# Kernel tuning notes

Measured on AMD Instinct MI355X. Metric: run time of the kernel, lower is better.

The kernel has to match this reference:

```python
import jax, jax.numpy as jnp
import numpy as np

DROP_I = 0.75  # input dropout prob
DROP_S = 0.25  # state dropout prob
DEPTH = 3      # recur_depth
NOISE_SEED = 42


def setup_inputs() -> dict:
    key = jax.random.key(0)
    ks = jax.random.split(key, 8)
    B, T, Din, D = 32, 2048, 512, 512
    s = 0.04  # init_scale
    u = lambda k, shape: jax.random.uniform(k, shape, jnp.float32, -s, s)
    return {
        "h0": jnp.zeros((1, D), jnp.float32),
        "seq": jax.random.normal(ks[0], (B, T, Din), jnp.float32),
        "wH": u(ks[1], (Din, D)),
        "bH": u(ks[2], (D,)),
        "wT": u(ks[3], (Din, D)),
        "bT": jnp.full((D,), -2.0, jnp.float32),  # init_T_bias
        "recurH_w": u(ks[4], (DEPTH, D, D)),
        # layer 0 has no bias in the source -> zero row is equivalent math
        "recurH_b": jnp.concatenate([jnp.zeros((1, D), jnp.float32), u(ks[5], (DEPTH - 1, D))], 0),
        "recurT_w": u(ks[6], (DEPTH, D, D)),
        "recurT_b": jnp.concatenate([jnp.zeros((1, D), jnp.float32), jnp.full((DEPTH - 1, D), -2.0, jnp.float32)], 0),
    }


def _dropout_noise(key, p_drop, shape, dtype):
    keep = 1.0 - p_drop
    return jax.random.bernoulli(key, keep, shape).astype(dtype) / keep


def _forward(h0, seq, wH, bH, wT, bT, recurH_w, recurH_b, recurT_w, recurT_b):
    B, T, Din = seq.shape
    D = wH.shape[1]
    k1, k2 = jax.random.split(jax.random.key(NOISE_SEED))
    # tied_noise=True: one input-noise mask shared by H/T paths, one state-noise mask
    noise_i = _dropout_noise(k1, DROP_I, (B, Din), seq.dtype)  # [B, Din], shared over time
    noise_s = _dropout_noise(k2, DROP_S, (B, D), seq.dtype)    # [B, D], shared over time & depth

    x = seq * noise_i[:, None, :]                              # [B, T, Din]
    i_H = jnp.einsum('btd,de->bte', x, wH) + bH                # [B, T, D]
    i_T = jnp.einsum('btd,de->bte', x, wT) + bT

    # Faithful to source: every timestep starts from H0 (state is not carried),
    # so time is a parallel axis and only the depth loop is sequential.
    s = jnp.broadcast_to(h0.reshape(1, 1, D), (B, T, D))
    for l in range(DEPTH):
        sd = s * noise_s[:, None, :]
        h_lin = jnp.einsum('btd,de->bte', sd, recurH_w[l]) + recurH_b[l]
        t_lin = jnp.einsum('btd,de->bte', sd, recurT_w[l]) + recurT_b[l]
        if l == 0:
            h_lin = h_lin + i_H
            t_lin = t_lin + i_T
        Hg = jnp.tanh(h_lin)
        Tg = jax.nn.sigmoid(t_lin)
        s = (Hg - s) * Tg + s  # highway combine
    return s  # [B, T, D]


def reference(h0, seq, wH, bH, wT, bT, recurH_w, recurH_b, recurT_w, recurT_b):
    return _forward(h0, seq, wH, bH, wT, bT, recurH_w, recurH_b, recurT_w, recurT_b)
```

## Files before the change

### kernel.cpp

```cpp
#include <hip/hip_runtime.h>
#include <stdint.h>
#include <math.h>

#define B_SZ   32
#define T_LEN  2048
#define DIN    512
#define DD     512
#define M_TOT  (B_SZ * T_LEN)
#define NTHREADS 256
#define WSZ    ((size_t)DD * DD)

typedef unsigned short u16;
typedef __attribute__((ext_vector_type(8))) short short8;
typedef __attribute__((ext_vector_type(4))) float f32x4;

__device__ __forceinline__ u16 f2bf(float f) {
  uint32_t u = __float_as_uint(f);
  uint32_t r = (u + 0x7FFFu + ((u >> 16) & 1u)) >> 16;
  return (u16)r;
}

typedef const void __attribute__((address_space(1)))* as1cp;
typedef void __attribute__((address_space(3)))* as3p;
__device__ __forceinline__ void async16(const void* g, void* l) {
  __builtin_amdgcn_global_load_lds((as1cp)(uintptr_t)g,
                                   (as3p)(uint32_t)(uintptr_t)l, 16, 0, 0);
}

__device__ __forceinline__ uint32_t rotl32(uint32_t x, int n) {
  return (x << n) | (x >> (32 - n));
}

__device__ __forceinline__ void threefry2x32(uint32_t k0, uint32_t k1,
                                             uint32_t x0, uint32_t x1,
                                             uint32_t& o0, uint32_t& o1) {
  const uint32_t ks0 = k0, ks1 = k1, ks2 = k0 ^ k1 ^ 0x1BD11BDAu;
  uint32_t v0 = x0 + ks0, v1 = x1 + ks1;
#define TF_R(r) { v0 += v1; v1 = rotl32(v1, (r)); v1 ^= v0; }
  TF_R(13) TF_R(15) TF_R(26) TF_R(6)
  v0 += ks1; v1 += ks2 + 1u;
  TF_R(17) TF_R(29) TF_R(16) TF_R(24)
  v0 += ks2; v1 += ks0 + 2u;
  TF_R(13) TF_R(15) TF_R(26) TF_R(6)
  v0 += ks0; v1 += ks1 + 3u;
  TF_R(17) TF_R(29) TF_R(16) TF_R(24)
  v0 += ks1; v1 += ks2 + 4u;
  TF_R(13) TF_R(15) TF_R(26) TF_R(6)
  v0 += ks2; v1 += ks0 + 5u;
#undef TF_R
  o0 = v0; o1 = v1;
}

__global__ void noise_kernel(float* __restrict__ noise_i, float* __restrict__ noise_s) {
  int i = blockIdx.x * blockDim.x + threadIdx.x;
  if (i >= B_SZ * DIN) return;
  uint32_t k1a, k1b, k2a, k2b;
  threefry2x32(0u, 42u, 0u, 0u, k1a, k1b);
  threefry2x32(0u, 42u, 0u, 1u, k2a, k2b);
  uint32_t b1, b2;
  threefry2x32(k1a, k1b, 0u, (uint32_t)i, b1, b2);
  noise_i[i] = (b1 < 0x40000000u) ? 4.0f : 0.0f;
  threefry2x32(k2a, k2b, 0u, (uint32_t)i, b1, b2);
  noise_s[i] = (b1 < 0xC0000000u) ? (1.0f / 0.75f) : 0.0f;
}

__global__ __launch_bounds__(256) void vec0_kernel(
    const float* __restrict__ h0, const float* __restrict__ noise_s,
    const float* __restrict__ rHw, const float* __restrict__ rHb,
    const float* __restrict__ rTw, const float* __restrict__ rTb,
    float* __restrict__ vH0, float* __restrict__ vT0) {
  __shared__ float sdv[DD];
  const int b = blockIdx.x >> 1;
  const int c = (blockIdx.x & 1) * 256 + threadIdx.x;
  for (int k = threadIdx.x; k < DD; k += 256)
    sdv[k] = h0[k] * noise_s[b * DD + k];
  __syncthreads();
  float aH = 0.f, aT = 0.f;
  for (int k = 0; k < DD; ++k) {
    float v = sdv[k];
    aH += v * rHw[(size_t)k * DD + c];
    aT += v * rTw[(size_t)k * DD + c];
  }
  vH0[b * DD + c] = aH + rHb[c];
  vT0[b * DD + c] = aT + rTb[c];
}

__global__ __launch_bounds__(256) void wt_all(
    const float* __restrict__ wH, const float* __restrict__ wT,
    const float* __restrict__ rHw, const float* __restrict__ rTw,
    u16* __restrict__ Wt) {
  __shared__ float tile[64][68];
  const int which = blockIdx.x >> 6;
  const float* W;
  switch (which) {
    case 0: W = wH; break;
    case 1: W = wT; break;
    case 2: W = rHw + WSZ; break;
    case 3: W = rTw + WSZ; break;
    case 4: W = rHw + 2 * WSZ; break;
    default: W = rTw + 2 * WSZ; break;
  }
  u16* dst = Wt + (size_t)which * WSZ;
  const int tb = blockIdx.x & 63;
  const int kt = (tb >> 3) * 64;
  const int nt = (tb & 7) * 64;
  const int tid = threadIdx.x;
  {
    int r = tid >> 2;
#pragma unroll
    for (int u = 0; u < 4; ++u) {
      int c = ((tid & 3) + u * 4) * 4;
      float4 v = *(const float4*)(W + (size_t)(kt + r) * DD + nt + c);
      tile[r][c] = v.x; tile[r][c + 1] = v.y; tile[r][c + 2] = v.z; tile[r][c + 3] = v.w;
    }
  }
  __syncthreads();
  {
    int n = tid >> 2, seg = (tid & 3) * 16;
    u16 o[16];
#pragma unroll
    for (int u = 0; u < 16; ++u) o[u] = f2bf(tile[seg + u][n]);
    *(uint4*)(dst + (size_t)(nt + n) * DD + kt + seg) = *(const uint4*)o;
    *(uint4*)(dst + (size_t)(nt + n) * DD + kt + seg + 8) = *(const uint4*)(o + 8);
  }
}

__global__ __launch_bounds__(256) void xprep(const float* __restrict__ seq,
                                             const float* __restrict__ noise_i,
                                             u16* __restrict__ Xbf) {
  int idx = blockIdx.x * 256 + threadIdx.x;
  int row = idx >> 6;
  int k8 = (idx & 63) * 8;
  int b = row >> 11;
  const float* s = seq + (size_t)row * DIN + k8;
  const float* n = noise_i + b * DIN + k8;
  float4 s0 = *(const float4*)s, s1 = *(const float4*)(s + 4);
  float4 n0 = *(const float4*)n, n1 = *(const float4*)(n + 4);
  u16 o[8];
  o[0] = f2bf(s0.x * n0.x); o[1] = f2bf(s0.y * n0.y);
  o[2] = f2bf(s0.z * n0.z); o[3] = f2bf(s0.w * n0.w);
  o[4] = f2bf(s1.x * n1.x); o[5] = f2bf(s1.y * n1.y);
  o[6] = f2bf(s1.z * n1.z); o[7] = f2bf(s1.w * n1.w);
  *(uint4*)(Xbf + (size_t)idx * 8) = *(const uint4*)o;
}

__global__ __launch_bounds__(256, 2) void layer_gemm(
    const u16* __restrict__ Abf,
    const u16* __restrict__ WtH,
    const u16* __restrict__ WtT,
    const float* __restrict__ hbv,
    const float* __restrict__ tbv,
    const float* __restrict__ vH0,
    const float* __restrict__ vT0,
    const float* __restrict__ h0,
    const float* __restrict__ noise_s,
    const float* Sprev,
    float* Snew,
    u16* __restrict__ SDnew,
    float* Out,
    int layer) {
  __shared__ u16 lds[24576];
  u16* ldsA  = lds;
  u16* ldsBH = lds + 8192;
  u16* ldsBT = lds + 16384;

  const int tid  = threadIdx.x;
  const int lane = tid & 63, wid = tid >> 6;
  const int bid  = blockIdx.x;
  const int m0   = (bid >> 2) * 128;
  const int c0   = (bid & 3) * 128;
  const int bidx = m0 >> 11;
  const int q  = lane >> 4, mr = lane & 15;
  const int wqm = wid >> 1, wqn = wid & 1;

  const u16* gA[4]; const u16* gBH[4]; const u16* gBT[4];
  u16* lA[4]; u16* lBH[4]; u16* lBT[4];
#pragma unroll
  for (int t = 0; t < 4; ++t) {
    int s  = wid * 256 + t * 64 + lane;
    int rm = s >> 3;
    int k8 = (s & 7) ^ (rm & 7);
    gA[t]  = Abf + (size_t)(m0 + rm) * DD + k8 * 8;
    gBH[t] = WtH + (size_t)(c0 + rm) * DD + k8 * 8;
    gBT[t] = WtT + (size_t)(c0 + rm) * DD + k8 * 8;
    int lofs = (wid * 256 + t * 64) * 8;
    lA[t] = ldsA + lofs; lBH[t] = ldsBH + lofs; lBT[t] = ldsBT + lofs;
  }

  f32x4 accH[4][4], accT[4][4];
#pragma unroll
  for (int i = 0; i < 4; ++i)
#pragma unroll
    for (int j = 0; j < 4; ++j) {
      accH[i][j] = (f32x4){0.f, 0.f, 0.f, 0.f};
      accT[i][j] = (f32x4){0.f, 0.f, 0.f, 0.f};
    }

  for (int kb = 0; kb < 8; ++kb) {
    __syncthreads();
    const int ko = kb * 64;
#pragma unroll
    for (int t = 0; t < 4; ++t) {
      async16(gA[t] + ko,  lA[t]);
      async16(gBH[t] + ko, lBH[t]);
      async16(gBT[t] + ko, lBT[t]);
    }
    __syncthreads();

#pragma unroll
    for (int ks = 0; ks < 2; ++ks) {
      const int jj = ((((ks << 2) + q) ^ (mr & 7)) << 3);
      short8 a[4];
#pragma unroll
      for (int mt = 0; mt < 4; ++mt)
        a[mt] = *(const short8*)(ldsA + (wqm * 64 + mt * 16 + mr) * 64 + jj);
#pragma unroll
      for (int nt = 0; nt < 4; ++nt) {
        int nofs = (wqn * 64 + nt * 16 + mr) * 64 + jj;
        short8 bh = *(const short8*)(ldsBH + nofs);
        short8 bt = *(const short8*)(ldsBT + nofs);
#pragma unroll
        for (int mt = 0; mt < 4; ++mt) {
          accH[mt][nt] = __builtin_amdgcn_mfma_f32_16x16x32_bf16(a[mt], bh, accH[mt][nt], 0, 0, 0);
          accT[mt][nt] = __builtin_amdgcn_mfma_f32_16x16x32_bf16(a[mt], bt, accT[mt][nt], 0, 0, 0);
        }
      }
    }
  }

  const int b512 = bidx * DD;
#pragma unroll
  for (int nt = 0; nt < 4; ++nt) {
    const int gc = c0 + wqn * 64 + nt * 16 + mr;
    float hb = hbv[gc], tb = tbv[gc];
    float nsc = 0.f, h0c = 0.f;
    if (layer == 0) {
      hb += vH0[b512 + gc];
      tb += vT0[b512 + gc];
      h0c = h0[gc];
    }
    if (layer < 2) nsc = noise_s[b512 + gc];
#pragma unroll
    for (int mt = 0; mt < 4; ++mt) {
      const int gmb = m0 + wqm * 64 + mt * 16 + q * 4;
#pragma unroll
      for (int r = 0; r < 4; ++r) {
        const size_t o = (size_t)(gmb + r) * DD + gc;
        float sp = (layer == 0) ? h0c : Sprev[o];
        float hg = tanhf(accH[mt][nt][r] + hb);
        float tg = 1.f / (1.f + __expf(-(accT[mt][nt][r] + tb)));
        float sn = (hg - sp) * tg + sp;
        if (layer < 2) {
          Snew[o] = sn;
          SDnew[o] = f2bf(sn * nsc);
        } else {
          Out[o] = sn;
        }
      }
    }
  }
}

extern "C" void kernel_launch(void* const* d_in, const int* in_sizes, int n_in,
                              void* d_out, int out_size, void* d_ws, size_t ws_size,
                              hipStream_t stream) {
  const float* h0  = (const float*)d_in[0];
  const float* seq = (const float*)d_in[1];
  const float* wH  = (const float*)d_in[2];
  const float* bH  = (const float*)d_in[3];
  const float* wT  = (const float*)d_in[4];
  const float* bT  = (const float*)d_in[5];
  const float* rHw = (const float*)d_in[6];
  const float* rHb = (const float*)d_in[7];
  const float* rTw = (const float*)d_in[8];
  const float* rTb = (const float*)d_in[9];
  float* out = (float*)d_out;

  char* ws = (char*)d_ws;
  float* noise_i = (float*)(ws);
  float* noise_s = (float*)(ws + (64 << 10));
  float* vH0     = (float*)(ws + (128 << 10));
  float* vT0     = (float*)(ws + (192 << 10));
  u16* Wt    = (u16*)(ws + (256 << 10));
  u16* Xbf   = (u16*)(ws + (4ull << 20));
  u16* SD0   = (u16*)(ws + (68ull << 20));

  noise_kernel<<<64, 256, 0, stream>>>(noise_i, noise_s);
  vec0_kernel<<<64, 256, 0, stream>>>(h0, noise_s, rHw, rHb, rTw, rTb, vH0, vT0);
  wt_all<<<384, 256, 0, stream>>>(wH, wT, rHw, rTw, Wt);
  xprep<<<M_TOT * DIN / 8 / 256, 256, 0, stream>>>(seq, noise_i, Xbf);

  const int NBLK = (M_TOT / 128) * (DD / 128);
  layer_gemm<<<NBLK, NTHREADS, 0, stream>>>(
      Xbf, Wt + 0 * WSZ, Wt + 1 * WSZ, bH, bT, vH0, vT0, h0, noise_s,
      nullptr, out, SD0, nullptr, 0);
  layer_gemm<<<NBLK, NTHREADS, 0, stream>>>(
      SD0, Wt + 2 * WSZ, Wt + 3 * WSZ, rHb + DD, rTb + DD, nullptr, nullptr, h0, noise_s,
      out, out, Xbf, nullptr, 1);
  layer_gemm<<<NBLK, NTHREADS, 0, stream>>>(
      Xbf, Wt + 4 * WSZ, Wt + 5 * WSZ, rHb + 2 * DD, rTb + 2 * DD, nullptr, nullptr, h0, noise_s,
      out, nullptr, nullptr, out, 2);
}
```

Before: 789.5 us.

## Triple-buffer K-loop with async LDS prefetch and swizzle block order

Replaces the single-buffered 64-wide K loop, which synchronized twice per step and waited on each load, with a 3-stage ring of 32-wide K tiles. Prefetching runs two tiles ahead and is gated by explicit vmcnt waits, so global-to-LDS copies overlap the MFMA work. It also remaps block IDs to change how tiles are spread across XCDs for L2 reuse. The cost is more LDS per block, which may affect occupancy, and the unswizzled LDS layout may introduce bank conflicts.

After: 801.4 us. Within noise of the previous version (+1.5%).

```diff
diff --git a/kernel.cpp b/kernel.cpp
--- a/kernel.cpp
+++ b/kernel.cpp
@@ -144,6 +144,9 @@
   *(uint4*)(Xbf + (size_t)idx * 8) = *(const uint4*)o;
 }
 
+#define WAITVM(n) asm volatile("s_waitcnt vmcnt(" #n ")" ::: "memory")
+#define WAITLG0() asm volatile("s_waitcnt lgkmcnt(0)" ::: "memory")
+
 __global__ __launch_bounds__(256, 2) void layer_gemm(
     const u16* __restrict__ Abf,
     const u16* __restrict__ WtH,
@@ -159,33 +162,38 @@
     u16* __restrict__ SDnew,
     float* Out,
     int layer) {
-  __shared__ u16 lds[24576];
-  u16* ldsA  = lds;
-  u16* ldsBH = lds + 8192;
-  u16* ldsBT = lds + 16384;
+  __shared__ u16 lds[36864];
 
   const int tid  = threadIdx.x;
   const int lane = tid & 63, wid = tid >> 6;
-  const int bid  = blockIdx.x;
+  const int bid  = (blockIdx.x & 7) * 256 + (blockIdx.x >> 3);
   const int m0   = (bid >> 2) * 128;
   const int c0   = (bid & 3) * 128;
   const int bidx = m0 >> 11;
   const int q  = lane >> 4, mr = lane & 15;
   const int wqm = wid >> 1, wqn = wid & 1;
 
-  const u16* gA[4]; const u16* gBH[4]; const u16* gBT[4];
-  u16* lA[4]; u16* lBH[4]; u16* lBT[4];
-#pragma unroll
-  for (int t = 0; t < 4; ++t) {
-    int s  = wid * 256 + t * 64 + lane;
-    int rm = s >> 3;
-    int k8 = (s & 7) ^ (rm & 7);
-    gA[t]  = Abf + (size_t)(m0 + rm) * DD + k8 * 8;
-    gBH[t] = WtH + (size_t)(c0 + rm) * DD + k8 * 8;
-    gBT[t] = WtT + (size_t)(c0 + rm) * DD + k8 * 8;
-    int lofs = (wid * 256 + t * 64) * 8;
-    lA[t] = ldsA + lofs; lBH[t] = ldsBH + lofs; lBT[t] = ldsBT + lofs;
-  }
+  const u16* gAb[2]; const u16* gBHb[2]; const u16* gBTb[2];
+  int lofs[2];
+#pragma unroll
+  for (int t = 0; t < 2; ++t) {
+    int g = tid + t * 256;
+    int row = g >> 2, k8 = (g & 3) * 8;
+    gAb[t]  = Abf + (size_t)(m0 + row) * DD + k8;
+    gBHb[t] = WtH + (size_t)(c0 + row) * DD + k8;
+    gBTb[t] = WtT + (size_t)(c0 + row) * DD + k8;
+    lofs[t] = g * 8;
+  }
+
+#define STAGE(bi, kb) do {                                     \
+    u16* ba = lds + (bi) * 12288;                              \
+    const int ko_ = (kb) * 32;                                 \
+    _Pragma("unroll")                                          \
+    for (int t = 0; t < 2; ++t) {                              \
+      async16(gAb[t]  + ko_, ba + lofs[t]);                    \
+      async16(gBHb[t] + ko_, ba + 4096 + lofs[t]);             \
+      async16(gBTb[t] + ko_, ba + 8192 + lofs[t]);             \
+    } } while (0)
 
   f32x4 accH[4][4], accT[4][4];
 #pragma unroll
@@ -196,37 +204,40 @@
       accT[i][j] = (f32x4){0.f, 0.f, 0.f, 0.f};
     }
 
-  for (int kb = 0; kb < 8; ++kb) {
-    __syncthreads();
-    const int ko = kb * 64;
-#pragma unroll
-    for (int t = 0; t < 4; ++t) {
-      async16(gA[t] + ko,  lA[t]);
-      async16(gBH[t] + ko, lBH[t]);
-      async16(gBT[t] + ko, lBT[t]);
-    }
-    __syncthreads();
-
-#pragma unroll
-    for (int ks = 0; ks < 2; ++ks) {
-      const int jj = ((((ks << 2) + q) ^ (mr & 7)) << 3);
-      short8 a[4];
-#pragma unroll
-      for (int mt = 0; mt < 4; ++mt)
-        a[mt] = *(const short8*)(ldsA + (wqm * 64 + mt * 16 + mr) * 64 + jj);
-#pragma unroll
-      for (int nt = 0; nt < 4; ++nt) {
-        int nofs = (wqn * 64 + nt * 16 + mr) * 64 + jj;
-        short8 bh = *(const short8*)(ldsBH + nofs);
-        short8 bt = *(const short8*)(ldsBT + nofs);
-#pragma unroll
-        for (int mt = 0; mt < 4; ++mt) {
-          accH[mt][nt] = __builtin_amdgcn_mfma_f32_16x16x32_bf16(a[mt], bh, accH[mt][nt], 0, 0, 0);
-          accT[mt][nt] = __builtin_amdgcn_mfma_f32_16x16x32_bf16(a[mt], bt, accT[mt][nt], 0, 0, 0);
-        }
+  STAGE(0, 0);
+  STAGE(1, 1);
+
+#pragma unroll
+  for (int kb = 0; kb < 16; ++kb) {
+    if (kb + 2 < 16) STAGE((kb + 2) % 3, kb + 2);
+    if (kb < 14)      WAITVM(12);
+    else if (kb == 14) WAITVM(6);
+    else               WAITVM(0);
+    __builtin_amdgcn_s_barrier();
+
+    const u16* bufA  = lds + (kb % 3) * 12288;
+    const u16* bufBH = bufA + 4096;
+    const u16* bufBT = bufA + 8192;
+
+    short8 a[4];
+#pragma unroll
+    for (int mt = 0; mt < 4; ++mt)
+      a[mt] = *(const short8*)(bufA + (wqm * 64 + mt * 16 + mr) * 32 + q * 8);
+#pragma unroll
+    for (int nt = 0; nt < 4; ++nt) {
+      const int nofs = (wqn * 64 + nt * 16 + mr) * 32 + q * 8;
+      short8 bh = *(const short8*)(bufBH + nofs);
+      short8 bt = *(const short8*)(bufBT + nofs);
+#pragma unroll
+      for (int mt = 0; mt < 4; ++mt) {
+        accH[mt][nt] = __builtin_amdgcn_mfma_f32_16x16x32_bf16(a[mt], bh, accH[mt][nt], 0, 0, 0);
+        accT[mt][nt] = __builtin_amdgcn_mfma_f32_16x16x32_bf16(a[mt], bt, accT[mt][nt], 0, 0, 0);
       }
     }
-  }
+    WAITLG0();
+    __builtin_amdgcn_s_barrier();
+  }
+#undef STAGE
 
   const int b512 = bidx * DD;
 #pragma unroll
```

## Fuse all three highway layers into one kernel with LDS-resident state

Applied to the files above, without the earlier changes.

Replaces the input-prep kernel and the three per-layer GEMM launches with one fused kernel. Each block keeps a 64-row fp32 state tile in LDS across all depth steps. The block loads seq asynchronously, applies the dropout noise and packs to bf16 on the fly when building A fragments, and streams weight fragments straight from global memory with register double-buffering. This removes the global round trips of the intermediate state and bf16 copies, and uses a fast exp-based tanh plus packed bf16 conversion. The trade-off is that weights are re-read from L2 by every block for every layer without LDS staging. The roughly 130KB LDS footprint also limits occupancy to about one 8-wave block per CU.

Result: slower. 1.321 ms (+67.4%).

```diff
diff --git a/kernel.cpp b/kernel.cpp
--- a/kernel.cpp
+++ b/kernel.cpp
@@ -7,17 +7,24 @@
 #define DIN    512
 #define DD     512
 #define M_TOT  (B_SZ * T_LEN)
-#define NTHREADS 256
+#define BM     64
 #define WSZ    ((size_t)DD * DD)
 
 typedef unsigned short u16;
 typedef __attribute__((ext_vector_type(8))) short short8;
 typedef __attribute__((ext_vector_type(4))) float f32x4;
+typedef __attribute__((ext_vector_type(4))) unsigned int u32x4;
 
 __device__ __forceinline__ u16 f2bf(float f) {
   uint32_t u = __float_as_uint(f);
   uint32_t r = (u + 0x7FFFu + ((u >> 16) & 1u)) >> 16;
   return (u16)r;
+}
+
+__device__ __forceinline__ uint32_t cvtpk(float lo, float hi) {
+  uint32_t r;
+  asm("v_cvt_pk_bf16_f32 %0, %1, %2" : "=v"(r) : "v"(lo), "v"(hi));
+  return r;
 }
 
 typedef const void __attribute__((address_space(1)))* as1cp;
@@ -25,6 +32,13 @@
 __device__ __forceinline__ void async16(const void* g, void* l) {
   __builtin_amdgcn_global_load_lds((as1cp)(uintptr_t)g,
                                    (as3p)(uint32_t)(uintptr_t)l, 16, 0, 0);
+}
+
+__device__ __forceinline__ float sigm_fast(float x) {
+  return 1.f / (1.f + __expf(-x));
+}
+__device__ __forceinline__ float tanh_fast(float x) {
+  return 1.f - 2.f / (1.f + __expf(2.f * x));
 }
 
 __device__ __forceinline__ uint32_t rotl32(uint32_t x, int n) {
@@ -125,139 +139,134 @@
   }
 }
 
-__global__ __launch_bounds__(256) void xprep(const float* __restrict__ seq,
-                                             const float* __restrict__ noise_i,
-                                             u16* __restrict__ Xbf) {
-  int idx = blockIdx.x * 256 + threadIdx.x;
-  int row = idx >> 6;
-  int k8 = (idx & 63) * 8;
-  int b = row >> 11;
-  const float* s = seq + (size_t)row * DIN + k8;
-  const float* n = noise_i + b * DIN + k8;
-  float4 s0 = *(const float4*)s, s1 = *(const float4*)(s + 4);
-  float4 n0 = *(const float4*)n, n1 = *(const float4*)(n + 4);
-  u16 o[8];
-  o[0] = f2bf(s0.x * n0.x); o[1] = f2bf(s0.y * n0.y);
-  o[2] = f2bf(s0.z * n0.z); o[3] = f2bf(s0.w * n0.w);
-  o[4] = f2bf(s1.x * n1.x); o[5] = f2bf(s1.y * n1.y);
-  o[6] = f2bf(s1.z * n1.z); o[7] = f2bf(s1.w * n1.w);
-  *(uint4*)(Xbf + (size_t)idx * 8) = *(const uint4*)o;
-}
-
-__global__ __launch_bounds__(256, 2) void layer_gemm(
-    const u16* __restrict__ Abf,
-    const u16* __restrict__ WtH,
-    const u16* __restrict__ WtT,
-    const float* __restrict__ hbv,
-    const float* __restrict__ tbv,
+__global__ __launch_bounds__(512, 2) void fused_rhn(
+    const float* __restrict__ seq,
+    const u16* __restrict__ Wt,
+    const float* __restrict__ noise_i,
+    const float* __restrict__ noise_s,
     const float* __restrict__ vH0,
     const float* __restrict__ vT0,
     const float* __restrict__ h0,
-    const float* __restrict__ noise_s,
-    const float* Sprev,
-    float* Snew,
-    u16* __restrict__ SDnew,
-    float* Out,
-    int layer) {
-  __shared__ u16 lds[24576];
-  u16* ldsA  = lds;
-  u16* ldsBH = lds + 8192;
-  u16* ldsBT = lds + 16384;
+    const float* __restrict__ bH, const float* __restrict__ bT,
+    const float* __restrict__ rHb, const float* __restrict__ rTb,
+    float* __restrict__ out) {
+  __shared__ float S[BM * DD];
+  __shared__ float nzi[DD];
+  __shared__ float nzs[DD];
 
   const int tid  = threadIdx.x;
   const int lane = tid & 63, wid = tid >> 6;
-  const int bid  = blockIdx.x;
-  const int m0   = (bid >> 2) * 128;
-  const int c0   = (bid & 3) * 128;
+  const int m0   = blockIdx.x * BM;
   const int bidx = m0 >> 11;
   const int q  = lane >> 4, mr = lane & 15;
-  const int wqm = wid >> 1, wqn = wid & 1;
-
-  const u16* gA[4]; const u16* gBH[4]; const u16* gBT[4];
-  u16* lA[4]; u16* lBH[4]; u16* lBT[4];
-#pragma unroll
-  for (int t = 0; t < 4; ++t) {
-    int s  = wid * 256 + t * 64 + lane;
-    int rm = s >> 3;
-    int k8 = (s & 7) ^ (rm & 7);
-    gA[t]  = Abf + (size_t)(m0 + rm) * DD + k8 * 8;
-    gBH[t] = WtH + (size_t)(c0 + rm) * DD + k8 * 8;
-    gBT[t] = WtT + (size_t)(c0 + rm) * DD + k8 * 8;
-    int lofs = (wid * 256 + t * 64) * 8;
-    lA[t] = ldsA + lofs; lBH[t] = ldsBH + lofs; lBT[t] = ldsBT + lofs;
-  }
-
-  f32x4 accH[4][4], accT[4][4];
-#pragma unroll
-  for (int i = 0; i < 4; ++i)
-#pragma unroll
-    for (int j = 0; j < 4; ++j) {
-      accH[i][j] = (f32x4){0.f, 0.f, 0.f, 0.f};
-      accT[i][j] = (f32x4){0.f, 0.f, 0.f, 0.f};
+  const int c0w = wid * 64;
+  const int swm = (mr & 7) << 4;
+
+  if (tid < DD) {
+    nzi[tid] = noise_i[bidx * DD + tid];
+    nzs[tid] = noise_s[bidx * DD + tid];
+  }
+#pragma unroll
+  for (int t = 0; t < 16; ++t) {
+    int g = tid + t * 512;
+    int row = g >> 7, slot = g & 127;
+    int j16 = slot ^ (row & 7);
+    async16(seq + (size_t)(m0 + row) * DD + j16 * 4, (char*)S + (size_t)g * 16);
+  }
+  __syncthreads();
+
+  for (int l = 0; l < 3; ++l) {
+    const u16* WH = Wt + (size_t)(2 * l) * WSZ;
+    const u16* WTm = WH + WSZ;
+    const float* nz = (l == 0) ? nzi : nzs;
+
+    f32x4 accH[4][4], accT[4][4];
+#pragma unroll
+    for (int i = 0; i < 4; ++i)
+#pragma unroll
+      for (int j = 0; j < 4; ++j) {
+        accH[i][j] = (f32x4){0.f, 0.f, 0.f, 0.f};
+        accT[i][j] = (f32x4){0.f, 0.f, 0.f, 0.f};
+      }
+
+    short8 wh[2][4], wt_[2][4];
+#pragma unroll
+    for (int nt = 0; nt < 4; ++nt) {
+      const size_t co = (size_t)(c0w + nt * 16 + mr) * DD + q * 8;
+      wh[0][nt]  = *(const short8*)(WH + co);
+      wt_[0][nt] = *(const short8*)(WTm + co);
     }
 
-  for (int kb = 0; kb < 8; ++kb) {
+#pragma unroll
+    for (int kb = 0; kb < 16; ++kb) {
+      const int cur = kb & 1, nxt = cur ^ 1;
+      if (kb < 15) {
+#pragma unroll
+        for (int nt = 0; nt < 4; ++nt) {
+          const size_t co = (size_t)(c0w + nt * 16 + mr) * DD + (kb + 1) * 32 + q * 8;
+          wh[nxt][nt]  = *(const short8*)(WH + co);
+          wt_[nxt][nt] = *(const short8*)(WTm + co);
+        }
+      }
+      const int k0 = kb * 32 + q * 8;
+      const float4 n0 = *(const float4*)&nz[k0];
+      const float4 n1 = *(const float4*)&nz[k0 + 4];
+      short8 a[4];
+#pragma unroll
+      for (int mt = 0; mt < 4; ++mt) {
+        const int row = mt * 16 + mr;
+        const char* Sb = (const char*)S + (size_t)row * 2048;
+        const int kbase = kb * 128 + q * 32;
+        float4 v0 = *(const float4*)(Sb + (kbase ^ swm));
+        float4 v1 = *(const float4*)(Sb + ((kbase + 16) ^ swm));
+        u32x4 pk;
+        pk.x = cvtpk(v0.x * n0.x, v0.y * n0.y);
+        pk.y = cvtpk(v0.z * n0.z, v0.w * n0.w);
+        pk.z = cvtpk(v1.x * n1.x, v1.y * n1.y);
+        pk.w = cvtpk(v1.z * n1.z, v1.w * n1.w);
+        a[mt] = *(short8*)&pk;
+      }
+#pragma unroll
+      for (int nt = 0; nt < 4; ++nt) {
+#pragma unroll
+        for (int mt = 0; mt < 4; ++mt) {
+          accH[mt][nt] = __builtin_amdgcn_mfma_f32_16x16x32_bf16(a[mt], wh[cur][nt],  accH[mt][nt], 0, 0, 0);
+          accT[mt][nt] = __builtin_amdgcn_mfma_f32_16x16x32_bf16(a[mt], wt_[cur][nt], accT[mt][nt], 0, 0, 0);
+        }
+      }
+    }
+
     __syncthreads();
-    const int ko = kb * 64;
-#pragma unroll
-    for (int t = 0; t < 4; ++t) {
-      async16(gA[t] + ko,  lA[t]);
-      async16(gBH[t] + ko, lBH[t]);
-      async16(gBT[t] + ko, lBT[t]);
+
+    const float* hbv = (l == 0) ? bH : (rHb + l * DD);
+    const float* tbv = (l == 0) ? bT : (rTb + l * DD);
+    const int b512 = bidx * DD;
+#pragma unroll
+    for (int nt = 0; nt < 4; ++nt) {
+      const int gc = c0w + nt * 16 + mr;
+      float hb = hbv[gc], tb = tbv[gc];
+      float h0c = 0.f;
+      if (l == 0) {
+        hb += vH0[b512 + gc];
+        tb += vT0[b512 + gc];
+        h0c = h0[gc];
+      }
+#pragma unroll
+      for (int mt = 0; mt < 4; ++mt) {
+#pragma unroll
+        for (int r = 0; r < 4; ++r) {
+          const int row = mt * 16 + q * 4 + r;
+          char* Sp = (char*)S + (size_t)row * 2048 + (((unsigned)(gc * 4)) ^ ((row & 7) << 4));
+          float sp = (l == 0) ? h0c : *(const float*)Sp;
+          float hg = tanh_fast(accH[mt][nt][r] + hb);
+          float tg = sigm_fast(accT[mt][nt][r] + tb);
+          float sn = (hg - sp) * tg + sp;
+          if (l < 2) *(float*)Sp = sn;
+          else out[(size_t)(m0 + row) * DD + gc] = sn;
+        }
+      }
     }
     __syncthreads();
-
-#pragma unroll
-    for (int ks = 0; ks < 2; ++ks) {
-      const int jj = ((((ks << 2) + q) ^ (mr & 7)) << 3);
-      short8 a[4];
-#pragma unroll
-      for (int mt = 0; mt < 4; ++mt)
-        a[mt] = *(const short8*)(ldsA + (wqm * 64 + mt * 16 + mr) * 64 + jj);
-#pragma unroll
-      for (int nt = 0; nt < 4; ++nt) {
-        int nofs = (wqn * 64 + nt * 16 + mr) * 64 + jj;
-        short8 bh = *(const short8*)(ldsBH + nofs);
-        short8 bt = *(const short8*)(ldsBT + nofs);
-#pragma unroll
-        for (int mt = 0; mt < 4; ++mt) {
-          accH[mt][nt] = __builtin_amdgcn_mfma_f32_16x16x32_bf16(a[mt], bh, accH[mt][nt], 0, 0, 0);
-          accT[mt][nt] = __builtin_amdgcn_mfma_f32_16x16x32_bf16(a[mt], bt, accT[mt][nt], 0, 0, 0);
-        }
-      }
-    }
-  }
-
-  const int b512 = bidx * DD;
-#pragma unroll
-  for (int nt = 0; nt < 4; ++nt) {
-    const int gc = c0 + wqn * 64 + nt * 16 + mr;
-    float hb = hbv[gc], tb = tbv[gc];
-    float nsc = 0.f, h0c = 0.f;
-    if (layer == 0) {
-      hb += vH0[b512 + gc];
-      tb += vT0[b512 + gc];
-      h0c = h0[gc];
-    }
-    if (layer < 2) nsc = noise_s[b512 + gc];
-#pragma unroll
-    for (int mt = 0; mt < 4; ++mt) {
-      const int gmb = m0 + wqm * 64 + mt * 16 + q * 4;
-#pragma unroll
-      for (int r = 0; r < 4; ++r) {
-        const size_t o = (size_t)(gmb + r) * DD + gc;
-        float sp = (layer == 0) ? h0c : Sprev[o];
-        float hg = tanhf(accH[mt][nt][r] + hb);
-        float tg = 1.f / (1.f + __expf(-(accT[mt][nt][r] + tb)));
-        float sn = (hg - sp) * tg + sp;
-        if (layer < 2) {
-          Snew[o] = sn;
-          SDnew[o] = f2bf(sn * nsc);
-        } else {
-          Out[o] = sn;
-        }
-      }
-    }
   }
 }
 
@@ -282,22 +291,11 @@
   float* vH0     = (float*)(ws + (128 << 10));
   float* vT0     = (float*)(ws + (192 << 10));
   u16* Wt    = (u16*)(ws + (256 << 10));
-  u16* Xbf   = (u16*)(ws + (4ull << 20));
-  u16* SD0   = (u16*)(ws + (68ull << 20));
 
   noise_kernel<<<64, 256, 0, stream>>>(noise_i, noise_s);
   vec0_kernel<<<64, 256, 0, stream>>>(h0, noise_s, rHw, rHb, rTw, rTb, vH0, vT0);
   wt_all<<<384, 256, 0, stream>>>(wH, wT, rHw, rTw, Wt);
-  xprep<<<M_TOT * DIN / 8 / 256, 256, 0, stream>>>(seq, noise_i, Xbf);
-
-  const int NBLK = (M_TOT / 128) * (DD / 128);
-  layer_gemm<<<NBLK, NTHREADS, 0, stream>>>(
-      Xbf, Wt + 0 * WSZ, Wt + 1 * WSZ, bH, bT, vH0, vT0, h0, noise_s,
-      nullptr, out, SD0, nullptr, 0);
-  layer_gemm<<<NBLK, NTHREADS, 0, stream>>>(
-      SD0, Wt + 2 * WSZ, Wt + 3 * WSZ, rHb + DD, rTb + DD, nullptr, nullptr, h0, noise_s,
-      out, out, Xbf, nullptr, 1);
-  layer_gemm<<<NBLK, NTHREADS, 0, stream>>>(
-      Xbf, Wt + 4 * WSZ, Wt + 5 * WSZ, rHb + 2 * DD, rTb + 2 * DD, nullptr, nullptr, h0, noise_s,
-      out, nullptr, nullptr, out, 2);
-}
+
+  fused_rhn<<<M_TOT / BM, 512, 0, stream>>>(
+      seq, Wt, noise_i, noise_s, vH0, vT0, h0, bH, bT, rHb, rTb, out);
+}
```
